# Performance work log

Hardware: AMD Instinct MI355X
Metric: run time of the kernel (lower is better)

## Reference

```python
import jax, jax.numpy as jnp
import numpy as np

SAMPLE_RATE = 24000
THRESHOLD_FACTOR = 5.0
MAX_SPIKE_SAMPLES = int(0.0015 * SAMPLE_RATE)  # 36
K_MAX = 65536  # static upper bound on number of threshold crossings
N_SAMPLES = 24_000_000


def setup_inputs() -> dict:
    key = jax.random.key(0)
    x = jax.random.normal(key, (N_SAMPLES,), dtype=jnp.float32)
    return {"data_detected": x}


def _detect_one(v, threshold):
    """Detect peaks of v above +threshold. For the negative pass, call with -x
    (x < -thr  <=>  -x > thr, and argmin(x) == argmax(-x)). Returns an int32
    array of length K_MAX: valid peak indices first (sorted), padded with -1."""
    N = v.shape[0]
    mask = (v > threshold).astype(jnp.int32)
    d = jnp.diff(mask)  # +1 = entry (False->True), -1 = exit (True->False)
    entries = jnp.nonzero(d == 1, size=K_MAX, fill_value=N)[0]
    exits = jnp.nonzero(d == -1, size=K_MAX, fill_value=N)[0]
    n = jnp.minimum(jnp.sum(d == 1), jnp.sum(d == -1))
    idx = jnp.arange(K_MAX)
    dur = exits - entries
    keep = (idx < n) & (dur <= MAX_SPIKE_SAMPLES)
    # vectorized windowed peak search: (K_MAX, W) gather + row argmax
    win_idx = jnp.clip(entries[:, None] + jnp.arange(MAX_SPIKE_SAMPLES)[None, :], 0, N - 1)
    windows = v[win_idx]
    peaks = entries + jnp.argmax(windows, axis=1)
    # compact valid peaks to the front (entries are sorted), pad with -1
    peaks = jnp.sort(jnp.where(keep, peaks, N))
    total = jnp.sum(keep)
    return jnp.where(idx < total, peaks, -1)


def reference(data_detected):
    x = data_detected
    threshold = THRESHOLD_FACTOR * jnp.median(jnp.abs(x)) / 0.6745
    pos_indices = _detect_one(x, threshold)
    neg_indices = _detect_one(-x, threshold)
    return pos_indices, neg_indices, threshold
```

## Files before the change

kernel.cpp:

```cpp
#include <hip/hip_runtime.h>
#include <stdint.h>

#define HIST2_BITS 18
#define HIST1_SIZE 8192
#define LOW18_MASK 0x3FFFF
#define CAND_CAP 8192
#define LIST_CAP 1500000
#define LBUF_CAP 3072
#define PAIR_CAP 1024
#define PEAK_CAP 512
#define MAX_SPIKE 36

#define P_B1    0
#define P_B2    1
#define P_R1    2
#define P_R2    3
#define P_THRLO 4
#define P_THR   5
#define P_CANDN 6
#define P_LISTN 7
#define P_BINA0 8
#define P_BINA1 9
#define P_RA0   10
#define P_RA1   11
#define P_TAG1  12

#define WS_HIST1   0
#define WS_HISTA   32768
#define WS_HISTB   40960
#define WS_PARAMS  43008
#define WS_TOTALS  43072
#define WS_ZERO_BYTES 43080
#define WS_CAND    65536
#define WS_PEAKSP  98304
#define WS_PEAKSN  100352
#define WS_LIST    102400

__global__ __launch_bounds__(256) void k_hist1(const float* __restrict__ x, int N,
                                               int* __restrict__ hist1) {
  __shared__ int h[HIST1_SIZE];
  for (int i = threadIdx.x; i < HIST1_SIZE; i += 256) h[i] = 0;
  __syncthreads();
  int NV = N >> 2;
  int str = gridDim.x * 256;
  int j = blockIdx.x * 256 + threadIdx.x;
  const float4* vec = reinterpret_cast<const float4*>(x);
  for (; j + str < NV; j += 2 * str) {
    float4 a = vec[j];
    float4 b = vec[j + str];
    atomicAdd(&h[(__float_as_uint(a.x) & 0x7fffffffu) >> HIST2_BITS], 1);
    atomicAdd(&h[(__float_as_uint(a.y) & 0x7fffffffu) >> HIST2_BITS], 1);
    atomicAdd(&h[(__float_as_uint(a.z) & 0x7fffffffu) >> HIST2_BITS], 1);
    atomicAdd(&h[(__float_as_uint(a.w) & 0x7fffffffu) >> HIST2_BITS], 1);
    atomicAdd(&h[(__float_as_uint(b.x) & 0x7fffffffu) >> HIST2_BITS], 1);
    atomicAdd(&h[(__float_as_uint(b.y) & 0x7fffffffu) >> HIST2_BITS], 1);
    atomicAdd(&h[(__float_as_uint(b.z) & 0x7fffffffu) >> HIST2_BITS], 1);
    atomicAdd(&h[(__float_as_uint(b.w) & 0x7fffffffu) >> HIST2_BITS], 1);
  }
  if (j < NV) {
    float4 a = vec[j];
    atomicAdd(&h[(__float_as_uint(a.x) & 0x7fffffffu) >> HIST2_BITS], 1);
    atomicAdd(&h[(__float_as_uint(a.y) & 0x7fffffffu) >> HIST2_BITS], 1);
    atomicAdd(&h[(__float_as_uint(a.z) & 0x7fffffffu) >> HIST2_BITS], 1);
    atomicAdd(&h[(__float_as_uint(a.w) & 0x7fffffffu) >> HIST2_BITS], 1);
  }
  if (blockIdx.x == 0 && threadIdx.x == 0) {
    for (int i = NV << 2; i < N; ++i)
      atomicAdd(&h[(__float_as_uint(x[i]) & 0x7fffffffu) >> HIST2_BITS], 1);
  }
  __syncthreads();
  for (int i = threadIdx.x; i < HIST1_SIZE; i += 256) {
    int c = h[i];
    if (c) atomicAdd(&hist1[i], c);
  }
}

__global__ void k_select(const int* __restrict__ hist1, long long k1, long long k2,
                         int* __restrict__ p) {
  __shared__ int part[256];
  __shared__ long long excl[256];
  __shared__ int b1s, b2s, cb1s, cb2s;
  int tid = threadIdx.x;
  const int chunk = HIST1_SIZE / 256;
  int base = tid * chunk;
  int s = 0;
  for (int w = 0; w < chunk; ++w) s += hist1[base + w];
  part[tid] = s;
  __syncthreads();
  if (tid == 0) {
    long long acc = 0;
    for (int i = 0; i < 256; ++i) { excl[i] = acc; acc += part[i]; }
  }
  __syncthreads();
  long long pre = excl[tid];
  if (pre <= k1 && k1 < pre + part[tid]) {
    long long acc = pre;
    for (int w = 0; w < chunk; ++w) {
      int c = hist1[base + w];
      if (k1 < acc + c) { b1s = base + w; cb1s = (int)(k1 - acc); break; }
      acc += c;
    }
  }
  if (pre <= k2 && k2 < pre + part[tid]) {
    long long acc = pre;
    for (int w = 0; w < chunk; ++w) {
      int c = hist1[base + w];
      if (k2 < acc + c) { b2s = base + w; cb2s = (int)(k2 - acc); break; }
      acc += c;
    }
  }
  __syncthreads();
  if (tid == 0) {
    p[P_B1] = b1s; p[P_B2] = b2s;
    p[P_R1] = cb1s; p[P_R2] = cb2s;
    float lo1 = __uint_as_float((uint32_t)b1s << HIST2_BITS);
    float lo2 = __uint_as_float((uint32_t)b2s << HIST2_BITS);
    float mLo = 0.5f * (lo1 + lo2);
    p[P_THRLO] = __float_as_int((5.0f * mLo / 0.6745f) * 0.999f);
  }
}

__device__ inline void p2_elem(float f, int idx, int b1, int b2, float thrLo,
                               int* lbuf, int* lcnt,
                               int* listN, int* list, int* p, int* cand) {
  uint32_t u = __float_as_uint(f) & 0x7fffffffu;
  int top = (int)(u >> HIST2_BITS);
  bool in1 = (top == b1);
  bool in2 = (top == b2) && !in1;
  if (in1 || in2) {
    int val = (in2 ? (1 << HIST2_BITS) : 0) | (int)(u & LOW18_MASK);
    int id = atomicAdd(lcnt, 1);
    if (id < LBUF_CAP) lbuf[id] = val;
    else { int g = atomicAdd(&p[P_LISTN], 1); if (g < LIST_CAP) list[g] = val; }
  }
  if (__uint_as_float(u) > thrLo) {
    int id = atomicAdd(&p[P_CANDN], 1);
    if (id < CAND_CAP) cand[id] = idx;
  }
}

__global__ __launch_bounds__(256) void k_pass2(const float* __restrict__ x, int N,
                                               int* __restrict__ p,
                                               int* __restrict__ list,
                                               int* __restrict__ cand) {
  __shared__ int lbuf[LBUF_CAP];
  __shared__ int lcnt;
  __shared__ int lbase;
  if (threadIdx.x == 0) lcnt = 0;
  __syncthreads();
  int b1 = p[P_B1], b2 = p[P_B2];
  float thrLo = __int_as_float(p[P_THRLO]);
  int NV = N >> 2;
  int str = gridDim.x * 256;
  int j = blockIdx.x * 256 + threadIdx.x;
  const float4* vec = reinterpret_cast<const float4*>(x);
  for (; j + str < NV; j += 2 * str) {
    float4 a = vec[j];
    float4 b = vec[j + str];
    int ba = j << 2, bb = (j + str) << 2;
    p2_elem(a.x, ba + 0, b1, b2, thrLo, lbuf, &lcnt, 0, list, p, cand);
    p2_elem(a.y, ba + 1, b1, b2, thrLo, lbuf, &lcnt, 0, list, p, cand);
    p2_elem(a.z, ba + 2, b1, b2, thrLo, lbuf, &lcnt, 0, list, p, cand);
    p2_elem(a.w, ba + 3, b1, b2, thrLo, lbuf, &lcnt, 0, list, p, cand);
    p2_elem(b.x, bb + 0, b1, b2, thrLo, lbuf, &lcnt, 0, list, p, cand);
    p2_elem(b.y, bb + 1, b1, b2, thrLo, lbuf, &lcnt, 0, list, p, cand);
    p2_elem(b.z, bb + 2, b1, b2, thrLo, lbuf, &lcnt, 0, list, p, cand);
    p2_elem(b.w, bb + 3, b1, b2, thrLo, lbuf, &lcnt, 0, list, p, cand);
  }
  if (j < NV) {
    float4 a = vec[j];
    int ba = j << 2;
    p2_elem(a.x, ba + 0, b1, b2, thrLo, lbuf, &lcnt, 0, list, p, cand);
    p2_elem(a.y, ba + 1, b1, b2, thrLo, lbuf, &lcnt, 0, list, p, cand);
    p2_elem(a.z, ba + 2, b1, b2, thrLo, lbuf, &lcnt, 0, list, p, cand);
    p2_elem(a.w, ba + 3, b1, b2, thrLo, lbuf, &lcnt, 0, list, p, cand);
  }
  if (blockIdx.x == 0 && threadIdx.x == 0) {
    for (int i = NV << 2; i < N; ++i)
      p2_elem(x[i], i, b1, b2, thrLo, lbuf, &lcnt, 0, list, p, cand);
  }
  __syncthreads();
  int n = lcnt < LBUF_CAP ? lcnt : LBUF_CAP;
  if (threadIdx.x == 0) lbase = atomicAdd(&p[P_LISTN], n);
  __syncthreads();
  int base = lbase;
  for (int i = threadIdx.x; i < n; i += 256)
    if (base + i < LIST_CAP) list[base + i] = lbuf[i];
}

__global__ __launch_bounds__(256) void k_histA(const int* __restrict__ list,
                                               const int* __restrict__ p,
                                               int* __restrict__ histA) {
  __shared__ int h[2048];
  for (int i = threadIdx.x; i < 2048; i += 256) h[i] = 0;
  __syncthreads();
  int n = p[P_LISTN]; if (n > LIST_CAP) n = LIST_CAP;
  int str = gridDim.x * 256;
  for (int i = blockIdx.x * 256 + threadIdx.x; i < n; i += str) {
    int v = list[i];
    int tag = (v >> HIST2_BITS) & 1;
    atomicAdd(&h[tag * 1024 + ((v >> 8) & 1023)], 1);
  }
  __syncthreads();
  for (int i = threadIdx.x; i < 2048; i += 256) {
    int c = h[i];
    if (c) atomicAdd(&histA[i], c);
  }
}

__global__ void k_selA(const int* __restrict__ histA, int* __restrict__ p) {
  __shared__ int sh[256];
  __shared__ int excl[256];
  int tid = threadIdx.x;
  int b1 = p[P_B1], b2 = p[P_B2];
  for (int tgt = 0; tgt < 2; ++tgt) {
    __syncthreads();
    int tag = (tgt == 1 && b1 != b2) ? 1 : 0;
    int rank = p[P_R1 + tgt];
    const int* h = histA + tag * 1024;
    int c0 = h[tid * 4], c1 = h[tid * 4 + 1], c2 = h[tid * 4 + 2], c3 = h[tid * 4 + 3];
    sh[tid] = c0 + c1 + c2 + c3;
    __syncthreads();
    if (tid == 0) {
      int a = 0;
      for (int i = 0; i < 256; ++i) { excl[i] = a; a += sh[i]; }
    }
    __syncthreads();
    int pre = excl[tid];
    if (pre <= rank && rank < pre + sh[tid]) {
      int a = pre;
      int cc[4] = {c0, c1, c2, c3};
      for (int w = 0; w < 4; ++w) {
        if (rank < a + cc[w]) {
          p[P_BINA0 + tgt] = tid * 4 + w;
          p[P_RA0 + tgt] = rank - a;
          if (tgt == 1) p[P_TAG1] = tag;
          break;
        }
        a += cc[w];
      }
    }
  }
}

__global__ __launch_bounds__(256) void k_histB(const int* __restrict__ list,
                                               const int* __restrict__ p,
                                               int* __restrict__ histB) {
  __shared__ int h[512];
  if (threadIdx.x < 512) h[threadIdx.x] = 0;
  __syncthreads();
  int n = p[P_LISTN]; if (n > LIST_CAP) n = LIST_CAP;
  int bA0 = p[P_BINA0], bA1 = p[P_BINA1], tag1 = p[P_TAG1];
  int str = gridDim.x * 256;
  for (int i = blockIdx.x * 256 + threadIdx.x; i < n; i += str) {
    int v = list[i];
    int tag = (v >> HIST2_BITS) & 1;
    int ba = (v >> 8) & 1023;
    int lo = v & 255;
    if (tag == 0 && ba == bA0) atomicAdd(&h[lo], 1);
    if (tag == tag1 && ba == bA1) atomicAdd(&h[256 + lo], 1);
  }
  __syncthreads();
  if (threadIdx.x < 512) {
    int c = h[threadIdx.x];
    if (c) atomicAdd(&histB[threadIdx.x], c);
  }
}

__global__ void k_thrF(const int* __restrict__ histB, int* __restrict__ p) {
  __shared__ int sh[256];
  __shared__ int excl[256];
  __shared__ float vres[2];
  int tid = threadIdx.x;
  int b1 = p[P_B1], b2 = p[P_B2];
  for (int tgt = 0; tgt < 2; ++tgt) {
    __syncthreads();
    const int* h = histB + tgt * 256;
    int rank = p[P_RA0 + tgt];
    int c = h[tid];
    sh[tid] = c;
    __syncthreads();
    if (tid == 0) {
      int a = 0;
      for (int i = 0; i < 256; ++i) { excl[i] = a; a += sh[i]; }
    }
    __syncthreads();
    int pre = excl[tid];
    if (pre <= rank && rank < pre + c) {
      int bkt = (tgt == 0) ? b1 : b2;
      uint32_t bits = ((uint32_t)bkt << HIST2_BITS) |
                      ((uint32_t)p[P_BINA0 + tgt] << 8) | (uint32_t)tid;
      vres[tgt] = __uint_as_float(bits);
    }
  }
  __syncthreads();
  if (tid == 0) {
    float med = 0.5f * (vres[0] + vres[1]);
    p[P_THR] = __float_as_int((5.0f * med) / 0.6745f);
  }
}

__device__ static void isort(int* a, int n) {
  for (int i = 1; i < n; ++i) {
    int v = a[i]; int j = i - 1;
    while (j >= 0 && a[j] > v) { a[j + 1] = a[j]; --j; }
    a[j + 1] = v;
  }
}

__device__ inline void eval_pair(const float* __restrict__ x, int p, float thr,
                                 int* pe, int* px, int* ne, int* nx, int* cnt) {
  float a = x[p], b = x[p + 1];
  bool m0 = a > thr, m1 = b > thr;
  if (m0 != m1) {
    int id = atomicAdd(&cnt[m1 ? 0 : 1], 1);
    if (id < PAIR_CAP) (m1 ? pe : px)[id] = p;
  }
  bool q0 = (-a) > thr, q1 = (-b) > thr;
  if (q0 != q1) {
    int id = atomicAdd(&cnt[q1 ? 2 : 3], 1);
    if (id < PAIR_CAP) (q1 ? ne : nx)[id] = p;
  }
}

__device__ inline int wave_argmax36(const float* __restrict__ x, int N, int sign,
                                    int e, int lane) {
  float val = -INFINITY;
  int wi = lane;
  if (lane < MAX_SPIKE) {
    int idx = e + lane; if (idx > N - 1) idx = N - 1;
    float v = x[idx];
    val = (sign < 0) ? -v : v;
  }
  for (int off = 32; off; off >>= 1) {
    float ov = __shfl_xor(val, off);
    int owi = __shfl_xor(wi, off);
    if (ov > val || (ov == val && owi < wi)) { val = ov; wi = owi; }
  }
  return e + wi;
}

__device__ inline int proc_pol(const float* __restrict__ x, int N, int sign,
                               const int* eL, int nE, const int* xL, int nX,
                               int* pk, int tid) {
  int n = nE < nX ? nE : nX;
  int tot = 0;
  for (int t = 0; t < n; ++t) {
    int dur = xL[t] - eL[t];
    if (dur <= MAX_SPIKE) {
      int pp = wave_argmax36(x, N, sign, eL[t], tid);
      if (tot < PEAK_CAP && tid == 0) pk[tot] = pp;
      ++tot;
    }
  }
  if (tot > PEAK_CAP) tot = PEAK_CAP;
  if (tid == 0) isort(pk, tot);
  return tot;
}

__global__ void k_finalize(const float* __restrict__ x, int N,
                           int* __restrict__ p, int* __restrict__ cand,
                           int* __restrict__ peaksP, int* __restrict__ peaksN,
                           int* __restrict__ totals) {
  __shared__ int pe[PAIR_CAP], px[PAIR_CAP], ne[PAIR_CAP], nx[PAIR_CAP];
  __shared__ int cnt[4];
  __shared__ int pkP[PEAK_CAP], pkN[PEAK_CAP];
  __shared__ int nPk[2];
  int tid = threadIdx.x;
  float thr = __int_as_float(p[P_THR]);
  int nC = p[P_CANDN]; if (nC > CAND_CAP) nC = CAND_CAP;
  if (tid < 4) cnt[tid] = 0;
  __syncthreads();
  if (tid == 0) isort(cand, nC);
  __syncthreads();
  for (int k = tid; k < nC; k += 64) {
    int c = cand[k];
    bool prevAdj = (k > 0) && (cand[k - 1] == c - 1);
    if (c > 0 && !prevAdj) eval_pair(x, c - 1, thr, pe, px, ne, nx, cnt);
    if (c <= N - 2) eval_pair(x, c, thr, pe, px, ne, nx, cnt);
  }
  __syncthreads();
  int nPE = min(cnt[0], PAIR_CAP), nPX = min(cnt[1], PAIR_CAP);
  int nNE = min(cnt[2], PAIR_CAP), nNX = min(cnt[3], PAIR_CAP);
  if (tid == 0) { isort(pe, nPE); isort(px, nPX); }
  else if (tid == 1) { isort(ne, nNE); isort(nx, nNX); }
  __syncthreads();
  int t0 = proc_pol(x, N, +1, pe, nPE, px, nPX, pkP, tid);
  int t1 = proc_pol(x, N, -1, ne, nNE, nx, nNX, pkN, tid);
  if (tid == 0) { nPk[0] = t0; nPk[1] = t1; totals[0] = t0; totals[1] = t1; }
  __syncthreads();
  for (int j = tid; j < nPk[0]; j += 64) peaksP[j] = pkP[j];
  for (int j = tid; j < nPk[1]; j += 64) peaksN[j] = pkN[j];
}

__global__ __launch_bounds__(256) void k_fill(float* __restrict__ out, int OUT_K,
                                              const int* __restrict__ peaksP,
                                              const int* __restrict__ peaksN,
                                              const int* __restrict__ totals,
                                              const int* __restrict__ p) {
  int j = blockIdx.x * 256 + threadIdx.x;
  if (j >= 2 * OUT_K + 1) return;
  if (j < OUT_K) {
    out[j] = (j < totals[0]) ? (float)peaksP[j] : -1.0f;
  } else if (j < 2 * OUT_K) {
    int jj = j - OUT_K;
    out[j] = (jj < totals[1]) ? (float)peaksN[jj] : -1.0f;
  } else {
    out[j] = __int_as_float(p[P_THR]);
  }
}

extern "C" void kernel_launch(void* const* d_in, const int* in_sizes, int n_in,
                              void* d_out, int out_size, void* d_ws, size_t ws_size,
                              hipStream_t stream) {
  const float* x = (const float*)d_in[0];
  int N = in_sizes[0];
  float* out = (float*)d_out;
  char* ws = (char*)d_ws;

  int* hist1  = (int*)(ws + WS_HIST1);
  int* histA  = (int*)(ws + WS_HISTA);
  int* histB  = (int*)(ws + WS_HISTB);
  int* params = (int*)(ws + WS_PARAMS);
  int* totals = (int*)(ws + WS_TOTALS);
  int* cand   = (int*)(ws + WS_CAND);
  int* peaksP = (int*)(ws + WS_PEAKSP);
  int* peaksN = (int*)(ws + WS_PEAKSN);
  int* list   = (int*)(ws + WS_LIST);

  hipMemsetAsync(d_ws, 0, WS_ZERO_BYTES, stream);

  long long k1 = (long long)(N / 2) - 1;
  long long k2 = (long long)(N / 2);

  k_hist1<<<2048, 256, 0, stream>>>(x, N, hist1);
  k_select<<<1, 256, 0, stream>>>(hist1, k1, k2, params);
  k_pass2<<<2048, 256, 0, stream>>>(x, N, params, list, cand);
  k_histA<<<64, 256, 0, stream>>>(list, params, histA);
  k_selA<<<1, 256, 0, stream>>>(histA, params);
  k_histB<<<64, 256, 0, stream>>>(list, params, histB);
  k_thrF<<<1, 256, 0, stream>>>(histB, params);
  k_finalize<<<1, 64, 0, stream>>>(x, N, params, cand, peaksP, peaksN, totals);
  int OUT_K = (out_size - 1) / 2;
  k_fill<<<(2 * OUT_K + 1 + 255) / 256, 256, 0, stream>>>(out, OUT_K, peaksP, peaksN,
                                                          totals, params);
}
```

Before: 151.2 us.

## Fuse histogram selection stages with last-block pattern and write output directly

Merges the radix-select histogram kernels and their single-block selection kernels into two kernels that use a done-counter so the last block performs the prefix search. Changes the list encoding to store the raw absolute bits and re-splits the low bits (8+10 instead of 10+8). Removes the separate fill kernel by padding the output up front and having finalize write peaks directly. Also unrolls the streaming passes to 8 float4 loads per iteration. This cuts several kernel launches and intermediate buffers, at the cost of threadfence/atomic coordination.

```diff
diff --git a/kernel.cpp b/kernel.cpp
--- a/kernel.cpp
+++ b/kernel.cpp
@@ -1,15 +1,15 @@
 #include <hip/hip_runtime.h>
 #include <stdint.h>
 
-#define HIST2_BITS 18
+#define HB 18
 #define HIST1_SIZE 8192
-#define LOW18_MASK 0x3FFFF
 #define CAND_CAP 8192
 #define LIST_CAP 1500000
 #define LBUF_CAP 3072
 #define PAIR_CAP 1024
 #define PEAK_CAP 512
 #define MAX_SPIKE 36
+#define STAGE_BLOCKS 128
 
 #define P_B1    0
 #define P_B2    1
@@ -23,18 +23,16 @@
 #define P_BINA1 9
 #define P_RA0   10
 #define P_RA1   11
-#define P_TAG1  12
+#define P_DONEA 12
+#define P_DONEB 13
 
 #define WS_HIST1   0
 #define WS_HISTA   32768
-#define WS_HISTB   40960
+#define WS_HISTB   34816
 #define WS_PARAMS  43008
-#define WS_TOTALS  43072
-#define WS_ZERO_BYTES 43080
-#define WS_CAND    65536
-#define WS_PEAKSP  98304
-#define WS_PEAKSN  100352
-#define WS_LIST    102400
+#define WS_ZERO_BYTES 43072
+#define WS_CAND    43072
+#define WS_LIST    76800
 
 __global__ __launch_bounds__(256) void k_hist1(const float* __restrict__ x, int N,
                                                int* __restrict__ hist1) {
@@ -43,30 +41,30 @@
   __syncthreads();
   int NV = N >> 2;
   int str = gridDim.x * 256;
+  const float4* vec = reinterpret_cast<const float4*>(x);
   int j = blockIdx.x * 256 + threadIdx.x;
-  const float4* vec = reinterpret_cast<const float4*>(x);
-  for (; j + str < NV; j += 2 * str) {
+  for (; j + 7 * str < NV; j += 8 * str) {
+    float4 v[8];
+#pragma unroll
+    for (int k = 0; k < 8; ++k) v[k] = vec[j + k * str];
+#pragma unroll
+    for (int k = 0; k < 8; ++k) {
+      atomicAdd(&h[(__float_as_uint(v[k].x) & 0x7fffffffu) >> HB], 1);
+      atomicAdd(&h[(__float_as_uint(v[k].y) & 0x7fffffffu) >> HB], 1);
+      atomicAdd(&h[(__float_as_uint(v[k].z) & 0x7fffffffu) >> HB], 1);
+      atomicAdd(&h[(__float_as_uint(v[k].w) & 0x7fffffffu) >> HB], 1);
+    }
+  }
+  for (; j < NV; j += str) {
     float4 a = vec[j];
-    float4 b = vec[j + str];
-    atomicAdd(&h[(__float_as_uint(a.x) & 0x7fffffffu) >> HIST2_BITS], 1);
-    atomicAdd(&h[(__float_as_uint(a.y) & 0x7fffffffu) >> HIST2_BITS], 1);
-    atomicAdd(&h[(__float_as_uint(a.z) & 0x7fffffffu) >> HIST2_BITS], 1);
-    atomicAdd(&h[(__float_as_uint(a.w) & 0x7fffffffu) >> HIST2_BITS], 1);
-    atomicAdd(&h[(__float_as_uint(b.x) & 0x7fffffffu) >> HIST2_BITS], 1);
-    atomicAdd(&h[(__float_as_uint(b.y) & 0x7fffffffu) >> HIST2_BITS], 1);
-    atomicAdd(&h[(__float_as_uint(b.z) & 0x7fffffffu) >> HIST2_BITS], 1);
-    atomicAdd(&h[(__float_as_uint(b.w) & 0x7fffffffu) >> HIST2_BITS], 1);
-  }
-  if (j < NV) {
-    float4 a = vec[j];
-    atomicAdd(&h[(__float_as_uint(a.x) & 0x7fffffffu) >> HIST2_BITS], 1);
-    atomicAdd(&h[(__float_as_uint(a.y) & 0x7fffffffu) >> HIST2_BITS], 1);
-    atomicAdd(&h[(__float_as_uint(a.z) & 0x7fffffffu) >> HIST2_BITS], 1);
-    atomicAdd(&h[(__float_as_uint(a.w) & 0x7fffffffu) >> HIST2_BITS], 1);
+    atomicAdd(&h[(__float_as_uint(a.x) & 0x7fffffffu) >> HB], 1);
+    atomicAdd(&h[(__float_as_uint(a.y) & 0x7fffffffu) >> HB], 1);
+    atomicAdd(&h[(__float_as_uint(a.z) & 0x7fffffffu) >> HB], 1);
+    atomicAdd(&h[(__float_as_uint(a.w) & 0x7fffffffu) >> HB], 1);
   }
   if (blockIdx.x == 0 && threadIdx.x == 0) {
     for (int i = NV << 2; i < N; ++i)
-      atomicAdd(&h[(__float_as_uint(x[i]) & 0x7fffffffu) >> HIST2_BITS], 1);
+      atomicAdd(&h[(__float_as_uint(x[i]) & 0x7fffffffu) >> HB], 1);
   }
   __syncthreads();
   for (int i = threadIdx.x; i < HIST1_SIZE; i += 256) {
@@ -79,7 +77,7 @@
                          int* __restrict__ p) {
   __shared__ int part[256];
   __shared__ long long excl[256];
-  __shared__ int b1s, b2s, cb1s, cb2s;
+  __shared__ int b1s, b2s, r1s, r2s;
   int tid = threadIdx.x;
   const int chunk = HIST1_SIZE / 256;
   int base = tid * chunk;
@@ -97,7 +95,7 @@
     long long acc = pre;
     for (int w = 0; w < chunk; ++w) {
       int c = hist1[base + w];
-      if (k1 < acc + c) { b1s = base + w; cb1s = (int)(k1 - acc); break; }
+      if (k1 < acc + c) { b1s = base + w; r1s = (int)(k1 - acc); break; }
       acc += c;
     }
   }
@@ -105,33 +103,29 @@
     long long acc = pre;
     for (int w = 0; w < chunk; ++w) {
       int c = hist1[base + w];
-      if (k2 < acc + c) { b2s = base + w; cb2s = (int)(k2 - acc); break; }
+      if (k2 < acc + c) { b2s = base + w; r2s = (int)(k2 - acc); break; }
       acc += c;
     }
   }
   __syncthreads();
   if (tid == 0) {
     p[P_B1] = b1s; p[P_B2] = b2s;
-    p[P_R1] = cb1s; p[P_R2] = cb2s;
-    float lo1 = __uint_as_float((uint32_t)b1s << HIST2_BITS);
-    float lo2 = __uint_as_float((uint32_t)b2s << HIST2_BITS);
+    p[P_R1] = r1s; p[P_R2] = r2s;
+    float lo1 = __uint_as_float((uint32_t)b1s << HB);
+    float lo2 = __uint_as_float((uint32_t)b2s << HB);
     float mLo = 0.5f * (lo1 + lo2);
     p[P_THRLO] = __float_as_int((5.0f * mLo / 0.6745f) * 0.999f);
   }
 }
 
 __device__ inline void p2_elem(float f, int idx, int b1, int b2, float thrLo,
-                               int* lbuf, int* lcnt,
-                               int* listN, int* list, int* p, int* cand) {
+                               int* lbuf, int* lcnt, int* list, int* p, int* cand) {
   uint32_t u = __float_as_uint(f) & 0x7fffffffu;
-  int top = (int)(u >> HIST2_BITS);
-  bool in1 = (top == b1);
-  bool in2 = (top == b2) && !in1;
-  if (in1 || in2) {
-    int val = (in2 ? (1 << HIST2_BITS) : 0) | (int)(u & LOW18_MASK);
+  int top = (int)(u >> HB);
+  if (top == b1 || top == b2) {
     int id = atomicAdd(lcnt, 1);
-    if (id < LBUF_CAP) lbuf[id] = val;
-    else { int g = atomicAdd(&p[P_LISTN], 1); if (g < LIST_CAP) list[g] = val; }
+    if (id < LBUF_CAP) lbuf[id] = (int)u;
+    else { int g = atomicAdd(&p[P_LISTN], 1); if (g < LIST_CAP) list[g] = (int)u; }
   }
   if (__uint_as_float(u) > thrLo) {
     int id = atomicAdd(&p[P_CANDN], 1);
@@ -152,32 +146,32 @@
   float thrLo = __int_as_float(p[P_THRLO]);
   int NV = N >> 2;
   int str = gridDim.x * 256;
+  const float4* vec = reinterpret_cast<const float4*>(x);
   int j = blockIdx.x * 256 + threadIdx.x;
-  const float4* vec = reinterpret_cast<const float4*>(x);
-  for (; j + str < NV; j += 2 * str) {
+  for (; j + 7 * str < NV; j += 8 * str) {
+    float4 v[8];
+#pragma unroll
+    for (int k = 0; k < 8; ++k) v[k] = vec[j + k * str];
+#pragma unroll
+    for (int k = 0; k < 8; ++k) {
+      int base = (j + k * str) << 2;
+      p2_elem(v[k].x, base + 0, b1, b2, thrLo, lbuf, &lcnt, list, p, cand);
+      p2_elem(v[k].y, base + 1, b1, b2, thrLo, lbuf, &lcnt, list, p, cand);
+      p2_elem(v[k].z, base + 2, b1, b2, thrLo, lbuf, &lcnt, list, p, cand);
+      p2_elem(v[k].w, base + 3, b1, b2, thrLo, lbuf, &lcnt, list, p, cand);
+    }
+  }
+  for (; j < NV; j += str) {
     float4 a = vec[j];
-    float4 b = vec[j + str];
-    int ba = j << 2, bb = (j + str) << 2;
-    p2_elem(a.x, ba + 0, b1, b2, thrLo, lbuf, &lcnt, 0, list, p, cand);
-    p2_elem(a.y, ba + 1, b1, b2, thrLo, lbuf, &lcnt, 0, list, p, cand);
-    p2_elem(a.z, ba + 2, b1, b2, thrLo, lbuf, &lcnt, 0, list, p, cand);
-    p2_elem(a.w, ba + 3, b1, b2, thrLo, lbuf, &lcnt, 0, list, p, cand);
-    p2_elem(b.x, bb + 0, b1, b2, thrLo, lbuf, &lcnt, 0, list, p, cand);
-    p2_elem(b.y, bb + 1, b1, b2, thrLo, lbuf, &lcnt, 0, list, p, cand);
-    p2_elem(b.z, bb + 2, b1, b2, thrLo, lbuf, &lcnt, 0, list, p, cand);
-    p2_elem(b.w, bb + 3, b1, b2, thrLo, lbuf, &lcnt, 0, list, p, cand);
-  }
-  if (j < NV) {
-    float4 a = vec[j];
-    int ba = j << 2;
-    p2_elem(a.x, ba + 0, b1, b2, thrLo, lbuf, &lcnt, 0, list, p, cand);
-    p2_elem(a.y, ba + 1, b1, b2, thrLo, lbuf, &lcnt, 0, list, p, cand);
-    p2_elem(a.z, ba + 2, b1, b2, thrLo, lbuf, &lcnt, 0, list, p, cand);
-    p2_elem(a.w, ba + 3, b1, b2, thrLo, lbuf, &lcnt, 0, list, p, cand);
+    int base = j << 2;
+    p2_elem(a.x, base + 0, b1, b2, thrLo, lbuf, &lcnt, list, p, cand);
+    p2_elem(a.y, base + 1, b1, b2, thrLo, lbuf, &lcnt, list, p, cand);
+    p2_elem(a.z, base + 2, b1, b2, thrLo, lbuf, &lcnt, list, p, cand);
+    p2_elem(a.w, base + 3, b1, b2, thrLo, lbuf, &lcnt, list, p, cand);
   }
   if (blockIdx.x == 0 && threadIdx.x == 0) {
     for (int i = NV << 2; i < N; ++i)
-      p2_elem(x[i], i, b1, b2, thrLo, lbuf, &lcnt, 0, list, p, cand);
+      p2_elem(x[i], i, b1, b2, thrLo, lbuf, &lcnt, list, p, cand);
   }
   __syncthreads();
   int n = lcnt < LBUF_CAP ? lcnt : LBUF_CAP;
@@ -188,43 +182,95 @@
     if (base + i < LIST_CAP) list[base + i] = lbuf[i];
 }
 
-__global__ __launch_bounds__(256) void k_histA(const int* __restrict__ list,
-                                               const int* __restrict__ p,
-                                               int* __restrict__ histA) {
-  __shared__ int h[2048];
-  for (int i = threadIdx.x; i < 2048; i += 256) h[i] = 0;
+__global__ __launch_bounds__(256) void k_stageA(const int* __restrict__ list,
+                                                int* __restrict__ p,
+                                                int* __restrict__ histA) {
+  __shared__ int h[512];
+  __shared__ int lastS;
+  __shared__ int sh[256];
+  __shared__ int excl[256];
+  for (int i = threadIdx.x; i < 512; i += 256) h[i] = 0;
   __syncthreads();
   int n = p[P_LISTN]; if (n > LIST_CAP) n = LIST_CAP;
+  int b1 = p[P_B1], b2 = p[P_B2];
   int str = gridDim.x * 256;
   for (int i = blockIdx.x * 256 + threadIdx.x; i < n; i += str) {
     int v = list[i];
-    int tag = (v >> HIST2_BITS) & 1;
-    atomicAdd(&h[tag * 1024 + ((v >> 8) & 1023)], 1);
+    int top = v >> HB;
+    int bin = (v >> 10) & 255;
+    if (top == b1) atomicAdd(&h[bin], 1);
+    if (top == b2) atomicAdd(&h[256 + bin], 1);
+  }
+  __syncthreads();
+  for (int i = threadIdx.x; i < 512; i += 256) {
+    int c = h[i];
+    if (c) atomicAdd(&histA[i], c);
+  }
+  __threadfence();
+  if (threadIdx.x == 0) lastS = (atomicAdd(&p[P_DONEA], 1) == (int)gridDim.x - 1);
+  __syncthreads();
+  if (!lastS) return;
+  __threadfence();
+  int tid = threadIdx.x;
+  for (int tgt = 0; tgt < 2; ++tgt) {
+    int rank = p[P_R1 + tgt];
+    int c = histA[tgt * 256 + tid];
+    sh[tid] = c;
+    __syncthreads();
+    if (tid == 0) { int a = 0; for (int i = 0; i < 256; ++i) { excl[i] = a; a += sh[i]; } }
+    __syncthreads();
+    int pre = excl[tid];
+    if (pre <= rank && rank < pre + c) {
+      p[P_BINA0 + tgt] = tid;
+      p[P_RA0 + tgt] = rank - pre;
+    }
+    __syncthreads();
+  }
+}
+
+__global__ __launch_bounds__(256) void k_stageB(const int* __restrict__ list,
+                                                int* __restrict__ p,
+                                                int* __restrict__ histB,
+                                                float* __restrict__ outThr) {
+  __shared__ int h[2048];
+  __shared__ int lastS;
+  __shared__ int sh[256];
+  __shared__ int excl[256];
+  __shared__ float vres[2];
+  for (int i = threadIdx.x; i < 2048; i += 256) h[i] = 0;
+  __syncthreads();
+  int n = p[P_LISTN]; if (n > LIST_CAP) n = LIST_CAP;
+  int b1 = p[P_B1], b2 = p[P_B2];
+  int bA0 = p[P_BINA0], bA1 = p[P_BINA1];
+  int str = gridDim.x * 256;
+  for (int i = blockIdx.x * 256 + threadIdx.x; i < n; i += str) {
+    int v = list[i];
+    int top = v >> HB;
+    int bin = (v >> 10) & 255;
+    int lo = v & 1023;
+    if (top == b1 && bin == bA0) atomicAdd(&h[lo], 1);
+    if (top == b2 && bin == bA1) atomicAdd(&h[1024 + lo], 1);
   }
   __syncthreads();
   for (int i = threadIdx.x; i < 2048; i += 256) {
     int c = h[i];
-    if (c) atomicAdd(&histA[i], c);
-  }
-}
-
-__global__ void k_selA(const int* __restrict__ histA, int* __restrict__ p) {
-  __shared__ int sh[256];
-  __shared__ int excl[256];
+    if (c) atomicAdd(&histB[i], c);
+  }
+  __threadfence();
+  if (threadIdx.x == 0) lastS = (atomicAdd(&p[P_DONEB], 1) == (int)gridDim.x - 1);
+  __syncthreads();
+  if (!lastS) return;
+  __threadfence();
   int tid = threadIdx.x;
-  int b1 = p[P_B1], b2 = p[P_B2];
+  if (tid < 2) vres[tid] = 0.0f;
   for (int tgt = 0; tgt < 2; ++tgt) {
     __syncthreads();
-    int tag = (tgt == 1 && b1 != b2) ? 1 : 0;
-    int rank = p[P_R1 + tgt];
-    const int* h = histA + tag * 1024;
-    int c0 = h[tid * 4], c1 = h[tid * 4 + 1], c2 = h[tid * 4 + 2], c3 = h[tid * 4 + 3];
+    int rank = p[P_RA0 + tgt];
+    const int* hh = histB + tgt * 1024;
+    int c0 = hh[tid * 4], c1 = hh[tid * 4 + 1], c2 = hh[tid * 4 + 2], c3 = hh[tid * 4 + 3];
     sh[tid] = c0 + c1 + c2 + c3;
     __syncthreads();
-    if (tid == 0) {
-      int a = 0;
-      for (int i = 0; i < 256; ++i) { excl[i] = a; a += sh[i]; }
-    }
+    if (tid == 0) { int a = 0; for (int i = 0; i < 256; ++i) { excl[i] = a; a += sh[i]; } }
     __syncthreads();
     int pre = excl[tid];
     if (pre <= rank && rank < pre + sh[tid]) {
@@ -232,72 +278,28 @@
       int cc[4] = {c0, c1, c2, c3};
       for (int w = 0; w < 4; ++w) {
         if (rank < a + cc[w]) {
-          p[P_BINA0 + tgt] = tid * 4 + w;
-          p[P_RA0 + tgt] = rank - a;
-          if (tgt == 1) p[P_TAG1] = tag;
+          int bkt = (tgt == 0) ? b1 : b2;
+          uint32_t bits = ((uint32_t)bkt << HB) | ((uint32_t)p[P_BINA0 + tgt] << 10) |
+                          (uint32_t)(tid * 4 + w);
+          vres[tgt] = __uint_as_float(bits);
           break;
         }
         a += cc[w];
       }
     }
   }
-}
-
-__global__ __launch_bounds__(256) void k_histB(const int* __restrict__ list,
-                                               const int* __restrict__ p,
-                                               int* __restrict__ histB) {
-  __shared__ int h[512];
-  if (threadIdx.x < 512) h[threadIdx.x] = 0;
-  __syncthreads();
-  int n = p[P_LISTN]; if (n > LIST_CAP) n = LIST_CAP;
-  int bA0 = p[P_BINA0], bA1 = p[P_BINA1], tag1 = p[P_TAG1];
-  int str = gridDim.x * 256;
-  for (int i = blockIdx.x * 256 + threadIdx.x; i < n; i += str) {
-    int v = list[i];
-    int tag = (v >> HIST2_BITS) & 1;
-    int ba = (v >> 8) & 1023;
-    int lo = v & 255;
-    if (tag == 0 && ba == bA0) atomicAdd(&h[lo], 1);
-    if (tag == tag1 && ba == bA1) atomicAdd(&h[256 + lo], 1);
-  }
-  __syncthreads();
-  if (threadIdx.x < 512) {
-    int c = h[threadIdx.x];
-    if (c) atomicAdd(&histB[threadIdx.x], c);
-  }
-}
-
-__global__ void k_thrF(const int* __restrict__ histB, int* __restrict__ p) {
-  __shared__ int sh[256];
-  __shared__ int excl[256];
-  __shared__ float vres[2];
-  int tid = threadIdx.x;
-  int b1 = p[P_B1], b2 = p[P_B2];
-  for (int tgt = 0; tgt < 2; ++tgt) {
-    __syncthreads();
-    const int* h = histB + tgt * 256;
-    int rank = p[P_RA0 + tgt];
-    int c = h[tid];
-    sh[tid] = c;
-    __syncthreads();
-    if (tid == 0) {
-      int a = 0;
-      for (int i = 0; i < 256; ++i) { excl[i] = a; a += sh[i]; }
-    }
-    __syncthreads();
-    int pre = excl[tid];
-    if (pre <= rank && rank < pre + c) {
-      int bkt = (tgt == 0) ? b1 : b2;
-      uint32_t bits = ((uint32_t)bkt << HIST2_BITS) |
-                      ((uint32_t)p[P_BINA0 + tgt] << 8) | (uint32_t)tid;
-      vres[tgt] = __uint_as_float(bits);
-    }
-  }
   __syncthreads();
   if (tid == 0) {
     float med = 0.5f * (vres[0] + vres[1]);
-    p[P_THR] = __float_as_int((5.0f * med) / 0.6745f);
-  }
+    float thr = (5.0f * med) / 0.6745f;
+    p[P_THR] = __float_as_int(thr);
+    *outThr = thr;
+  }
+}
+
+__global__ __launch_bounds__(256) void k_fillpad(float* __restrict__ out, int n2) {
+  int j = blockIdx.x * 256 + threadIdx.x;
+  if (j < n2) out[j] = -1.0f;
 }
 
 __device__ static void isort(int* a, int n) {
@@ -360,8 +362,7 @@
 
 __global__ void k_finalize(const float* __restrict__ x, int N,
                            int* __restrict__ p, int* __restrict__ cand,
-                           int* __restrict__ peaksP, int* __restrict__ peaksN,
-                           int* __restrict__ totals) {
+                           float* __restrict__ out, int OUT_K) {
   __shared__ int pe[PAIR_CAP], px[PAIR_CAP], ne[PAIR_CAP], nx[PAIR_CAP];
   __shared__ int cnt[4];
   __shared__ int pkP[PEAK_CAP], pkN[PEAK_CAP];
@@ -387,27 +388,10 @@
   __syncthreads();
   int t0 = proc_pol(x, N, +1, pe, nPE, px, nPX, pkP, tid);
   int t1 = proc_pol(x, N, -1, ne, nNE, nx, nNX, pkN, tid);
-  if (tid == 0) { nPk[0] = t0; nPk[1] = t1; totals[0] = t0; totals[1] = t1; }
-  __syncthreads();
-  for (int j = tid; j < nPk[0]; j += 64) peaksP[j] = pkP[j];
-  for (int j = tid; j < nPk[1]; j += 64) peaksN[j] = pkN[j];
-}
-
-__global__ __launch_bounds__(256) void k_fill(float* __restrict__ out, int OUT_K,
-                                              const int* __restrict__ peaksP,
-                                              const int* __restrict__ peaksN,
-                                              const int* __restrict__ totals,
-                                              const int* __restrict__ p) {
-  int j = blockIdx.x * 256 + threadIdx.x;
-  if (j >= 2 * OUT_K + 1) return;
-  if (j < OUT_K) {
-    out[j] = (j < totals[0]) ? (float)peaksP[j] : -1.0f;
-  } else if (j < 2 * OUT_K) {
-    int jj = j - OUT_K;
-    out[j] = (jj < totals[1]) ? (float)peaksN[jj] : -1.0f;
-  } else {
-    out[j] = __int_as_float(p[P_THR]);
-  }
+  if (tid == 0) { nPk[0] = t0; nPk[1] = t1; }
+  __syncthreads();
+  for (int j = tid; j < nPk[0]; j += 64) out[j] = (float)pkP[j];
+  for (int j = tid; j < nPk[1]; j += 64) out[OUT_K + j] = (float)pkN[j];
 }
 
 extern "C" void kernel_launch(void* const* d_in, const int* in_sizes, int n_in,
@@ -422,26 +406,20 @@
   int* histA  = (int*)(ws + WS_HISTA);
   int* histB  = (int*)(ws + WS_HISTB);
   int* params = (int*)(ws + WS_PARAMS);
-  int* totals = (int*)(ws + WS_TOTALS);
   int* cand   = (int*)(ws + WS_CAND);
-  int* peaksP = (int*)(ws + WS_PEAKSP);
-  int* peaksN = (int*)(ws + WS_PEAKSN);
   int* list   = (int*)(ws + WS_LIST);
 
   hipMemsetAsync(d_ws, 0, WS_ZERO_BYTES, stream);
 
   long long k1 = (long long)(N / 2) - 1;
   long long k2 = (long long)(N / 2);
-
+  int OUT_K = (out_size - 1) / 2;
+
+  k_fillpad<<<(2 * OUT_K + 255) / 256, 256, 0, stream>>>(out, 2 * OUT_K);
   k_hist1<<<2048, 256, 0, stream>>>(x, N, hist1);
   k_select<<<1, 256, 0, stream>>>(hist1, k1, k2, params);
   k_pass2<<<2048, 256, 0, stream>>>(x, N, params, list, cand);
-  k_histA<<<64, 256, 0, stream>>>(list, params, histA);
-  k_selA<<<1, 256, 0, stream>>>(histA, params);
-  k_histB<<<64, 256, 0, stream>>>(list, params, histB);
-  k_thrF<<<1, 256, 0, stream>>>(histB, params);
-  k_finalize<<<1, 64, 0, stream>>>(x, N, params, cand, peaksP, peaksN, totals);
-  int OUT_K = (out_size - 1) / 2;
-  k_fill<<<(2 * OUT_K + 1 + 255) / 256, 256, 0, stream>>>(out, OUT_K, peaksP, peaksN,
-                                                          totals, params);
-}
+  k_stageA<<<STAGE_BLOCKS, 256, 0, stream>>>(list, params, histA);
+  k_stageB<<<STAGE_BLOCKS, 256, 0, stream>>>(list, params, histB, out + 2 * OUT_K);
+  k_finalize<<<1, 64, 0, stream>>>(x, N, params, cand, out, OUT_K);
+}
```

Result: slower. 160.4 us (+6.1%).
